# Performance work log

Hardware: AMD Instinct MI355X
Metric: run time of the kernel (lower is better)

Reference implementation:

```python
import jax, jax.numpy as jnp
import numpy as np

# Module constants (from init_kwargs)
NOISE_NUM = 64
SAMPLE_NUM = 262144
FCL = 65                 # filter_coeff_length
FL = 64                  # frame_length
GAIN = 1.0               # attenuate_gain
FRAME_NUM = SAMPLE_NUM // FL + 1   # 4097
IR = 2 * FCL - 1         # 129, linear-phase IR length
CONV = IR + FL - 1       # 192, per-frame filtered length
LOG10 = float(np.log(10.0))


def modified_sigmoid(x):
    # DDSP modified sigmoid: 2*sigmoid(x)^log(10) + 1e-7
    return 2.0 * jax.nn.sigmoid(x) ** LOG10 + 1e-7


def setup_inputs() -> dict:
    key = jax.random.key(0)
    k1, k2 = jax.random.split(key)
    coefficient_bank = jax.random.uniform(k1, (NOISE_NUM, FRAME_NUM, FCL),
                                          dtype=jnp.float32, minval=-1.0, maxval=1.0)
    noise = jax.random.uniform(k2, (NOISE_NUM, FRAME_NUM, FL), dtype=jnp.float32)
    return {"coefficient_bank": coefficient_bank, "noise": noise}


def reference(coefficient_bank, noise):
    B, F, L = coefficient_bank.shape  # (64, 4097, 65)
    # Zero-phase frequency response -> impulse response
    fr = modified_sigmoid(coefficient_bank)                  # (B,F,L) real half-spectrum
    zp_ir = jnp.fft.irfft(fr, n=IR, axis=-1)                 # (B,F,129)
    lp_ir = jnp.roll(zp_ir, L - 1, axis=-1)                  # linear phase
    # periodic hann window of length IR (torch.hann_window periodic=True)
    win = 0.5 * (1.0 - jnp.cos(2.0 * jnp.pi * jnp.arange(IR, dtype=jnp.float32) / IR))
    wir = lp_ir * win
    # FFT-domain filtering of per-frame noise (linear convolution length CONV)
    H = jnp.fft.rfft(jnp.pad(wir, ((0, 0), (0, 0), (0, FL - 1))), axis=-1)   # (B,F,97)
    n = noise * 2.0 - 1.0                                                    # uniform [-1,1)
    N = jnp.fft.rfft(jnp.pad(n, ((0, 0), (0, 0), (0, IR - 1))), axis=-1)     # (B,F,97)
    filtered = jnp.fft.irfft(N * H, n=CONV, axis=-1) * GAIN                  # (B,F,192)
    # Overlap-add with hop FL (replaces conv_transpose1d with identity kernel)
    total = (F - 1) * FL + CONV
    idx = (jnp.arange(F)[:, None] * FL + jnp.arange(CONV)[None, :]).reshape(-1)
    out = jnp.zeros((B, total), dtype=filtered.dtype).at[:, idx].add(filtered.reshape(B, -1))
    return out[:, :SAMPLE_NUM]
```

## Files before the change

### kernel.cpp

```cpp
#include <hip/hip_runtime.h>


#define NB 64
#define FTOT 4097
#define FCL 65
#define FL 64
#define SAMPLES 262144
#define OUT_FRAMES 4096
#define G 16
#define NF (G + 2)
#define NSTRIDE 68
#define PW 260
#define BLOCKS_PER_B (OUT_FRAMES / G)

__device__ __forceinline__ float mod_sigmoid(float x) {
    float s = 1.0f / (1.0f + __expf(-x));
    return 2.0f * __expf(2.302585092994046f * __logf(s)) + 1e-7f;
}

__device__ __forceinline__ float rdlane(float v, int k) {
    return __int_as_float(__builtin_amdgcn_readlane(__float_as_int(v), k));
}

__global__ __launch_bounds__(128) void fn_kernel(
    const float* __restrict__ coeff,
    const float* __restrict__ noise,
    float* __restrict__ out)
{
    __shared__ __align__(16) float costab[132];
    __shared__ __align__(16) float nS[NF * NSTRIDE];
    __shared__ __align__(16) float wirP[NF * PW];

    const int tid  = threadIdx.x;
    const int lane = tid & 63;
    const int wv   = tid >> 6;
    const int blk  = blockIdx.x;
    const int b    = blk / BLOCKS_PER_B;
    const int cg   = blk % BLOCKS_PER_B;
    const int fp0  = cg * G;
    const int fbase = fp0 - 2;

    for (int i = tid; i < NF * PW / 4; i += 128)
        ((float4*)wirP)[i] = make_float4(0.f, 0.f, 0.f, 0.f);
    for (int i = tid; i < 129; i += 128)
        costab[i] = __cosf(6.283185307179586f * (float)i * (1.0f / 129.0f));

    for (int i = tid; i < NF * 16; i += 128) {
        int q = i >> 4, g = i & 15;
        int f = fbase + q;
        float4 v = make_float4(0.f, 0.f, 0.f, 0.f);
        if (f >= 0) {
            const float4* src = (const float4*)(noise + ((size_t)b * FTOT + f) * FL);
            float4 u = src[g];
            v = make_float4(2.f*u.x-1.f, 2.f*u.y-1.f, 2.f*u.z-1.f, 2.f*u.w-1.f);
        }
        *(float4*)&nS[q * NSTRIDE + 4 * g] = v;
    }

    float frv[9], f64v[9];
    #pragma unroll
    for (int i = 0; i < 9; ++i) {
        int f = fbase + wv + 2 * i;
        if (f < 0) f = 0;
        const float* row = coeff + ((size_t)b * FTOT + f) * FCL;
        frv[i]  = row[lane];
        f64v[i] = row[64];
    }
    #pragma unroll
    for (int i = 0; i < 9; ++i) {
        frv[i]  = mod_sigmoid(frv[i]);
        f64v[i] = mod_sigmoid(f64v[i]);
    }

    __syncthreads();

    {
        float c  = costab[lane];
        float c2 = 2.0f * c;
        float cp = 1.0f;
        float ck = c;
        float S[9];
        #pragma unroll
        for (int i = 0; i < 9; ++i) S[i] = 0.5f * rdlane(frv[i], 0);
        #pragma unroll 8
        for (int k = 1; k < 64; ++k) {
            #pragma unroll
            for (int i = 0; i < 9; ++i)
                S[i] = __builtin_fmaf(rdlane(frv[i], k), ck, S[i]);
            float cn = __builtin_fmaf(c2, ck, -cp);
            cp = ck; ck = cn;
        }
        #pragma unroll
        for (int i = 0; i < 9; ++i)
            S[i] = __builtin_fmaf(f64v[i], ck, S[i]);
        float w1f = 0.5f - 0.5f * costab[64 + lane];
        float w2f = 0.5f - 0.5f * costab[64 - lane];
        #pragma unroll
        for (int i = 0; i < 9; ++i) {
            int fi = wv + 2 * i;
            float zp = S[i] * (2.0f / 129.0f);
            wirP[fi * PW + 127 + lane] = w1f * zp;
            wirP[fi * PW + 127 - lane] = w2f * zp;
        }
    }
    __syncthreads();

    {
        const int chunk = tid >> 3;
        const int r0    = (tid & 7) * 8;
        float a[8];
        #pragma unroll
        for (int j = 0; j < 8; ++j) a[j] = 0.0f;

        #pragma unroll
        for (int dd = 0; dd < 3; ++dd) {
            const int q = chunk + 2 - dd;
            const float* wb = &wirP[q * PW + 63 + 64 * dd + r0];
            const float4* n4p = (const float4*)&nS[q * NSTRIDE];
            float4 W1 = *(const float4*)(wb + 1);
            float4 W2 = *(const float4*)(wb + 5);
            #pragma unroll
            for (int s4 = 0; s4 < 16; ++s4) {
                float4 W0 = *(const float4*)(wb - 3 - 4 * s4);
                float4 n4 = n4p[s4];
                float w[11] = {W0.x, W0.y, W0.z, W0.w,
                               W1.x, W1.y, W1.z, W1.w,
                               W2.x, W2.y, W2.z};
                float nv[4] = {n4.x, n4.y, n4.z, n4.w};
                #pragma unroll
                for (int i = 0; i < 4; ++i)
                    #pragma unroll
                    for (int j = 0; j < 8; ++j)
                        a[j] = __builtin_fmaf(nv[i], w[j - i + 3], a[j]);
                W2 = W1; W1 = W0;
            }
        }

        float* op = &out[(size_t)b * SAMPLES + (size_t)fp0 * 64 + (size_t)tid * 8];
        *(float4*)op       = make_float4(a[0], a[1], a[2], a[3]);
        *(float4*)(op + 4) = make_float4(a[4], a[5], a[6], a[7]);
    }
}

extern "C" void kernel_launch(void* const* d_in, const int* in_sizes, int n_in,
                              void* d_out, int out_size, void* d_ws, size_t ws_size,
                              hipStream_t stream) {
    const float* coeff = (const float*)d_in[0];
    const float* noise = (const float*)d_in[1];
    float* out = (float*)d_out;
    dim3 grid(NB * BLOCKS_PER_B);
    fn_kernel<<<grid, 128, 0, stream>>>(coeff, noise, out);
}
```

Baseline: 293.2 us.

## Use packed fp16 dot2 for frame convolution with reversed half-precision IR tables

```diff
diff --git a/kernel.cpp b/kernel.cpp
--- a/kernel.cpp
+++ b/kernel.cpp
@@ -1,5 +1,7 @@
 #include <hip/hip_runtime.h>
 
+
+typedef __fp16 half2_t __attribute__((ext_vector_type(2)));
 
 #define NB 64
 #define FTOT 4097
@@ -9,8 +11,8 @@
 #define OUT_FRAMES 4096
 #define G 16
 #define NF (G + 2)
-#define NSTRIDE 68
-#define PW 260
+#define NSH 36
+#define PWH 264
 #define BLOCKS_PER_B (OUT_FRAMES / G)
 
 __device__ __forceinline__ float mod_sigmoid(float x) {
@@ -28,8 +30,9 @@
     float* __restrict__ out)
 {
     __shared__ __align__(16) float costab[132];
-    __shared__ __align__(16) float nS[NF * NSTRIDE];
-    __shared__ __align__(16) float wirP[NF * PW];
+    __shared__ __align__(16) half2_t nH[NF * NSH];
+    __shared__ __align__(16) __fp16 wrevA[NF * PWH];
+    __shared__ __align__(16) __fp16 wrevB[NF * PWH];
 
     const int tid  = threadIdx.x;
     const int lane = tid & 63;
@@ -40,21 +43,23 @@
     const int fp0  = cg * G;
     const int fbase = fp0 - 2;
 
-    for (int i = tid; i < NF * PW / 4; i += 128)
-        ((float4*)wirP)[i] = make_float4(0.f, 0.f, 0.f, 0.f);
+    for (int i = tid; i < (NF * PWH) / 8; i += 128) {
+        ((float4*)wrevA)[i] = make_float4(0.f, 0.f, 0.f, 0.f);
+        ((float4*)wrevB)[i] = make_float4(0.f, 0.f, 0.f, 0.f);
+    }
     for (int i = tid; i < 129; i += 128)
         costab[i] = __cosf(6.283185307179586f * (float)i * (1.0f / 129.0f));
 
     for (int i = tid; i < NF * 16; i += 128) {
         int q = i >> 4, g = i & 15;
         int f = fbase + q;
-        float4 v = make_float4(0.f, 0.f, 0.f, 0.f);
-        if (f >= 0) {
-            const float4* src = (const float4*)(noise + ((size_t)b * FTOT + f) * FL);
-            float4 u = src[g];
-            v = make_float4(2.f*u.x-1.f, 2.f*u.y-1.f, 2.f*u.z-1.f, 2.f*u.w-1.f);
-        }
-        *(float4*)&nS[q * NSTRIDE + 4 * g] = v;
+        float4 u = make_float4(0.5f, 0.5f, 0.5f, 0.5f);
+        if (f >= 0)
+            u = ((const float4*)(noise + ((size_t)b * FTOT + f) * FL))[g];
+        half2_t h0 = __builtin_amdgcn_cvt_pkrtz(2.f*u.x-1.f, 2.f*u.y-1.f);
+        half2_t h1 = __builtin_amdgcn_cvt_pkrtz(2.f*u.z-1.f, 2.f*u.w-1.f);
+        nH[q * NSH + 2 * g]     = h0;
+        nH[q * NSH + 2 * g + 1] = h1;
     }
 
     float frv[9], f64v[9];
@@ -99,46 +104,50 @@
         for (int i = 0; i < 9; ++i) {
             int fi = wv + 2 * i;
             float zp = S[i] * (2.0f / 129.0f);
-            wirP[fi * PW + 127 + lane] = w1f * zp;
-            wirP[fi * PW + 127 - lane] = w2f * zp;
+            __fp16 h1 = (__fp16)(w1f * zp);
+            __fp16 h2 = (__fp16)(w2f * zp);
+            wrevA[fi * PWH + 127 - lane] = h1;
+            wrevA[fi * PWH + 127 + lane] = h2;
+            wrevB[fi * PWH + 128 - lane] = h1;
+            wrevB[fi * PWH + 128 + lane] = h2;
         }
     }
     __syncthreads();
 
     {
         const int chunk = tid >> 3;
-        const int r0    = (tid & 7) * 8;
-        float a[8];
+        const int tf    = tid & 7;
+        const int par   = tf & 1;
+        const int r0    = (tf >> 1) * 16 + par;
+        float acc[8];
         #pragma unroll
-        for (int j = 0; j < 8; ++j) a[j] = 0.0f;
+        for (int i = 0; i < 8; ++i) acc[i] = 0.0f;
 
         #pragma unroll
         for (int dd = 0; dd < 3; ++dd) {
-            const int q = chunk + 2 - dd;
-            const float* wb = &wirP[q * PW + 63 + 64 * dd + r0];
-            const float4* n4p = (const float4*)&nS[q * NSTRIDE];
-            float4 W1 = *(const float4*)(wb + 1);
-            float4 W2 = *(const float4*)(wb + 5);
+            const int q  = chunk + 2 - dd;
+            const int C0 = 63 + 64 * dd + r0;
+            const __fp16* wr = (C0 & 1) ? &wrevB[q * PWH] : &wrevA[q * PWH];
+            const int h0 = ((C0 & 1) ? (255 - C0) : (254 - C0)) >> 1;
+            const half2_t* wrh  = (const half2_t*)wr;
+            const half2_t* nrow = &nH[q * NSH];
+
+            half2_t W[8];
             #pragma unroll
-            for (int s4 = 0; s4 < 16; ++s4) {
-                float4 W0 = *(const float4*)(wb - 3 - 4 * s4);
-                float4 n4 = n4p[s4];
-                float w[11] = {W0.x, W0.y, W0.z, W0.w,
-                               W1.x, W1.y, W1.z, W1.w,
-                               W2.x, W2.y, W2.z};
-                float nv[4] = {n4.x, n4.y, n4.z, n4.w};
+            for (int j = 0; j < 7; ++j) W[j] = wrh[h0 - 7 + j];
+            #pragma unroll
+            for (int t = 0; t < 32; ++t) {
+                W[(t + 7) & 7] = wrh[h0 + t];
+                half2_t a = nrow[t];
                 #pragma unroll
-                for (int i = 0; i < 4; ++i)
-                    #pragma unroll
-                    for (int j = 0; j < 8; ++j)
-                        a[j] = __builtin_fmaf(nv[i], w[j - i + 3], a[j]);
-                W2 = W1; W1 = W0;
+                for (int i = 0; i < 8; ++i)
+                    acc[i] = __builtin_amdgcn_fdot2(a, W[(t + 7 - i) & 7], acc[i], false);
             }
         }
 
-        float* op = &out[(size_t)b * SAMPLES + (size_t)fp0 * 64 + (size_t)tid * 8];
-        *(float4*)op       = make_float4(a[0], a[1], a[2], a[3]);
-        *(float4*)(op + 4) = make_float4(a[4], a[5], a[6], a[7]);
+        float* op = out + (size_t)b * SAMPLES + (size_t)(fp0 + chunk) * 64 + r0;
+        #pragma unroll
+        for (int i = 0; i < 8; ++i) op[2 * i] = acc[i];
     }
 }
 
```

After: 293.3 us. About the same (+0.0%).
